# Performance work log

Measured on AMD Instinct MI355X. Metric: run time of the kernel, lower is better.

Reference implementation:

```python
import jax, jax.numpy as jnp
import numpy as np

B, S = 16, 512
IN_DIM, ATTN_DIM, DEPTH, HEADS, DH = 512, 512, 4, 8, 64
CB_DIM, CB_SIZE, MAX_SEQ = 64, 8192, 544


def _ln(x, g, b):
    mu = x.mean(-1, keepdims=True)
    v = ((x - mu) ** 2).mean(-1, keepdims=True)
    return (x - mu) / jnp.sqrt(v + 1e-5) * g + b


def setup_inputs() -> dict:
    key = jax.random.key(0)
    ks = jax.random.split(key, 16)
    sc = 0.02
    d = {
        "x": jax.random.normal(ks[0], (B, S, IN_DIM), jnp.float32),
        "w_in": jax.random.normal(ks[1], (IN_DIM, ATTN_DIM), jnp.float32) * sc,
        "b_in": jnp.zeros((ATTN_DIM,), jnp.float32),
        "pos_emb": jax.random.normal(ks[2], (MAX_SEQ, ATTN_DIM), jnp.float32) * sc,
        "ln1_g": jnp.ones((DEPTH, ATTN_DIM), jnp.float32),
        "ln1_b": jnp.zeros((DEPTH, ATTN_DIM), jnp.float32),
        "wq": jax.random.normal(ks[3], (DEPTH, ATTN_DIM, ATTN_DIM), jnp.float32) * sc,
        "wk": jax.random.normal(ks[4], (DEPTH, ATTN_DIM, ATTN_DIM), jnp.float32) * sc,
        "wv": jax.random.normal(ks[5], (DEPTH, ATTN_DIM, ATTN_DIM), jnp.float32) * sc,
        "wo": jax.random.normal(ks[6], (DEPTH, ATTN_DIM, ATTN_DIM), jnp.float32) * sc,
        "ln2_g": jnp.ones((DEPTH, ATTN_DIM), jnp.float32),
        "ln2_b": jnp.zeros((DEPTH, ATTN_DIM), jnp.float32),
        "ff_w1": jax.random.normal(ks[7], (DEPTH, ATTN_DIM, 4 * ATTN_DIM), jnp.float32) * sc,
        "ff_b1": jnp.zeros((DEPTH, 4 * ATTN_DIM), jnp.float32),
        "ff_w2": jax.random.normal(ks[8], (DEPTH, 4 * ATTN_DIM, ATTN_DIM), jnp.float32) * sc,
        "ff_b2": jnp.zeros((DEPTH, ATTN_DIM), jnp.float32),
        "lnf_g": jnp.ones((ATTN_DIM,), jnp.float32),
        "lnf_b": jnp.zeros((ATTN_DIM,), jnp.float32),
        "w_out": jax.random.normal(ks[9], (ATTN_DIM, CB_DIM), jnp.float32) * sc,
        "b_out": jnp.zeros((CB_DIM,), jnp.float32),
        "codebook": jax.random.normal(ks[10], (CB_SIZE, CB_DIM), jnp.float32),
    }
    return d


def _attn(h, wq, wk, wv, wo):
    b, s, _ = h.shape
    q = jnp.einsum('bsd,de->bse', h, wq).reshape(b, s, HEADS, DH)
    k = jnp.einsum('bsd,de->bse', h, wk).reshape(b, s, HEADS, DH)
    v = jnp.einsum('bsd,de->bse', h, wv).reshape(b, s, HEADS, DH)
    scores = jnp.einsum('bqhd,bkhd->bhqk', q, k) * (DH ** -0.5)
    a = jax.nn.softmax(scores, axis=-1)
    o = jnp.einsum('bhqk,bkhd->bqhd', a, v).reshape(b, s, ATTN_DIM)
    return jnp.einsum('bse,ed->bsd', o, wo)


def reference(x, w_in, b_in, pos_emb, ln1_g, ln1_b, wq, wk, wv, wo,
              ln2_g, ln2_b, ff_w1, ff_b1, ff_w2, ff_b2, lnf_g, lnf_b,
              w_out, b_out, codebook):
    s = x.shape[1]
    # ContinuousTransformerWrapper: project in + absolute pos emb
    h = jnp.einsum('bsd,de->bse', x, w_in) + b_in + pos_emb[:s]
    # pre-norm encoder layers: attn + ff, each residual
    for i in range(DEPTH):
        h = h + _attn(_ln(h, ln1_g[i], ln1_b[i]), wq[i], wk[i], wv[i], wo[i])
        g = _ln(h, ln2_g[i], ln2_b[i])
        g = jax.nn.gelu(jnp.einsum('bsd,df->bsf', g, ff_w1[i]) + ff_b1[i])
        h = h + jnp.einsum('bsf,fd->bsd', g, ff_w2[i]) + ff_b2[i]
    h = _ln(h, lnf_g, lnf_b)
    z = jnp.einsum('bsd,dc->bsc', h, w_out) + b_out  # [B,S,CB_DIM]
    # VectorQuantize: euclidean nearest codebook entry
    d2 = (z ** 2).sum(-1, keepdims=True) - 2.0 * jnp.einsum('bsc,kc->bsk', z, codebook) \
         + (codebook ** 2).sum(-1)  # [B,S,CB_SIZE]
    idx = jnp.argmin(d2, axis=-1)
    q = codebook[idx]  # [B,S,CB_DIM]
    commit_loss = jnp.mean((jax.lax.stop_gradient(q) - z) ** 2)  # commitment_weight=1.0
    q_st = z + jax.lax.stop_gradient(q - z)  # straight-through
    return q_st.sum(axis=1), commit_loss
```

## Files before the change

kernel.cpp:

```cpp
#include <hip/hip_runtime.h>
#include <cmath>

#define BATCH 16
#define SEQ 512
#define DMODEL 512
#define NDEPTH 4
#define NHEADS 8
#define DHEAD 64
#define DFF 2048
#define CBD 64
#define CBS 8192
#define MROWS (BATCH * SEQ)

typedef unsigned short u16;
typedef __attribute__((ext_vector_type(8))) short short8;
typedef __attribute__((ext_vector_type(4))) float f32x4;
typedef __attribute__((ext_vector_type(4))) unsigned short u16x4;

__device__ __forceinline__ u16 f2bf(float f) {
    unsigned u = __float_as_uint(f);
    u += 0x7fff + ((u >> 16) & 1);
    return (u16)(u >> 16);
}
__device__ __forceinline__ float bf2f(u16 h) {
    return __uint_as_float(((unsigned)h) << 16);
}

__device__ __forceinline__ void async16(u16* lds, const u16* g) {
    __builtin_amdgcn_global_load_lds(
        (const __attribute__((address_space(1))) unsigned int*)g,
        (__attribute__((address_space(3))) unsigned int*)lds, 16, 0, 0);
}

__device__ __forceinline__ float gelu_tanh(float u) {
    float t = fmaf(0.07135481627f * u, u * u, 1.5957691216f * u);
    return u / (1.0f + __expf(-t));
}

__global__ void zero_kernel(float* __restrict__ p, int n) {
    int i = blockIdx.x * 256 + threadIdx.x;
    if (i < n) p[i] = 0.0f;
}

__global__ void cbn_kernel(const float* __restrict__ cb, float* __restrict__ cbn) {
    int c = blockIdx.x * 256 + threadIdx.x;
    if (c >= CBS) return;
    const float* row = cb + (size_t)c * CBD;
    float s = 0.0f;
#pragma unroll
    for (int d = 0; d < CBD; ++d) s += row[d] * row[d];
    cbn[c] = s;
}

__global__ __launch_bounds__(256) void wtrans_kernel(
    const float* __restrict__ W, u16* __restrict__ Th, u16* __restrict__ Tl,
    int K, int N, long inLS, long outLS) {
    __shared__ float t[32][33];
    const float* Ws = W + (size_t)blockIdx.z * inLS;
    u16* Tho = Th + (size_t)blockIdx.z * outLS;
    u16* Tlo = Tl + (size_t)blockIdx.z * outLS;
    int n0 = blockIdx.x * 32, k0 = blockIdx.y * 32;
    int tx = threadIdx.x & 31, ty = threadIdx.x >> 5;
#pragma unroll
    for (int r = ty; r < 32; r += 8) t[r][tx] = Ws[(size_t)(k0 + r) * N + n0 + tx];
    __syncthreads();
#pragma unroll
    for (int r = ty; r < 32; r += 8) {
        float v = t[tx][r];
        size_t o = (size_t)(n0 + r) * K + k0 + tx;
        u16 hh = f2bf(v);
        Tho[o] = hh;
        Tlo[o] = f2bf(v - bf2f(hh));
    }
}

__global__ __launch_bounds__(256) void vtrans_kernel(
    const u16* __restrict__ Qh, const u16* __restrict__ Ql,
    u16* __restrict__ VTh, u16* __restrict__ VTl) {
    __shared__ u16 t[64][68];
    int s0 = blockIdx.x * 64;
    int hh = blockIdx.y;
    int b = blockIdx.z & 15, plane = blockIdx.z >> 4;
    const u16* src = (plane ? Ql : Qh) + ((size_t)(16 + hh) * MROWS) * 64;
    u16* dst = (plane ? VTl : VTh);
    int tid = threadIdx.x;
    int rr = tid >> 4, c4 = (tid & 15) * 4;
#pragma unroll
    for (int i = 0; i < 4; ++i) {
        int r = rr + i * 16;
        const u16* p = src + (size_t)(b * SEQ + s0 + r) * 64 + c4;
        *(u16x4*)(&t[r][c4]) = *(const u16x4*)p;
    }
    __syncthreads();
#pragma unroll
    for (int i = 0; i < 4; ++i) {
        int r = rr + i * 16;
        u16x4 v;
        v.x = t[c4 + 0][r]; v.y = t[c4 + 1][r]; v.z = t[c4 + 2][r]; v.w = t[c4 + 3][r];
        *(u16x4*)(dst + (size_t)b * SEQ * DMODEL + (size_t)(hh * 64 + r) * SEQ + s0 + c4) = v;
    }
}

__global__ void split_kernel(const float* __restrict__ X, u16* __restrict__ H,
                             u16* __restrict__ L, int n) {
    int i = blockIdx.x * 256 + threadIdx.x;
    if (i < n) {
        float v = X[i];
        u16 hh = f2bf(v);
        H[i] = hh;
        L[i] = f2bf(v - bf2f(hh));
    }
}

__global__ __launch_bounds__(256) void ln_kernel(
    const float* __restrict__ X,
    const float* __restrict__ C0, const float* __restrict__ C1,
    const float* __restrict__ bias2, const float* __restrict__ pos2,
    float* __restrict__ Xout,
    float* __restrict__ Y, u16* __restrict__ Yh, u16* __restrict__ Yl,
    const float* __restrict__ g, const float* __restrict__ b) {
    int row  = blockIdx.x * 4 + (threadIdx.x >> 6);
    int lane = threadIdx.x & 63;
    float v[8];
    float s = 0.0f;
#pragma unroll
    for (int j = 0; j < 8; ++j) {
        int d = lane + j * 64;
        size_t o = (size_t)row * DMODEL + d;
        float t = X ? X[o] : 0.0f;
        if (C0)    t += C0[o] + C1[o];
        if (bias2) t += bias2[d];
        if (pos2)  t += pos2[(size_t)(row & (SEQ - 1)) * DMODEL + d];
        v[j] = t;
        if (Xout) Xout[o] = t;
        s += t;
    }
#pragma unroll
    for (int off = 32; off; off >>= 1) s += __shfl_xor(s, off);
    float mu  = s * (1.0f / DMODEL);
    float var = 0.0f;
#pragma unroll
    for (int j = 0; j < 8; ++j) { float d = v[j] - mu; var += d * d; }
#pragma unroll
    for (int off = 32; off; off >>= 1) var += __shfl_xor(var, off);
    float r = rsqrtf(var * (1.0f / DMODEL) + 1e-5f);
#pragma unroll
    for (int j = 0; j < 8; ++j) {
        int d = lane + j * 64;
        float y = (v[j] - mu) * r * g[d] + b[d];
        size_t o = (size_t)row * DMODEL + d;
        if (Y) Y[o] = y;
        if (Yh) {
            u16 hh = f2bf(y);
            Yh[o] = hh;
            Yl[o] = f2bf(y - bf2f(hh));
        }
    }
}

__global__ __launch_bounds__(256) void gemm3_kernel(
    const u16* __restrict__ Ah, const u16* __restrict__ Al,
    const u16* __restrict__ Bh, const u16* __restrict__ Bl,
    float* __restrict__ Cf, u16* __restrict__ Ch, u16* __restrict__ Cl,
    const float* __restrict__ bias, const float* __restrict__ res,
    const float* __restrict__ pos, int M, int N, int K, int gelu,
    float* __restrict__ Cs0, float* __restrict__ Cs1, int kslice, int qkvscatter) {
    __shared__ __align__(16) u16 AsH[128 * 64];
    __shared__ __align__(16) u16 AsL[128 * 64];
    __shared__ __align__(16) u16 BsH[128 * 64];
    __shared__ __align__(16) u16 BsL[128 * 64];

    int tid  = threadIdx.x;
    int w    = tid >> 6, lane = tid & 63;
    int wr   = w >> 1, wc = w & 1;
    int quad = lane >> 4, l16 = lane & 15;
    int m0   = blockIdx.x * 128;
    int n0   = blockIdx.y * 128;
    int ksA  = (kslice > 0) ? blockIdx.z * kslice : 0;
    int ksB  = (kslice > 0) ? ksA + kslice : K;

    f32x4 acc[4][4];
#pragma unroll
    for (int i = 0; i < 4; ++i)
#pragma unroll
        for (int j = 0; j < 4; ++j) acc[i][j] = (f32x4){0.f, 0.f, 0.f, 0.f};

    int ldsoff[4];
    size_t goff[4];
#pragma unroll
    for (int r = 0; r < 4; ++r) {
        int cidx = tid + 256 * r;
        int row = cidx >> 3;
        int cg = (cidx & 7) ^ (row & 7);
        ldsoff[r] = cidx * 8;
        goff[r] = (size_t)row * K + cg * 8;
    }

    const u16* AbaseH = Ah + (size_t)m0 * K;
    const u16* AbaseL = Al + (size_t)m0 * K;
    const u16* BbaseH = Bh + (size_t)n0 * K;
    const u16* BbaseL = Bl + (size_t)n0 * K;

    for (int ks = ksA; ks < ksB; ks += 64) {
        __syncthreads();
#pragma unroll
        for (int r = 0; r < 4; ++r) {
            size_t g = goff[r] + ks;
            async16(&AsH[ldsoff[r]], AbaseH + g);
            async16(&AsL[ldsoff[r]], AbaseL + g);
            async16(&BsH[ldsoff[r]], BbaseH + g);
            async16(&BsL[ldsoff[r]], BbaseL + g);
        }
        __syncthreads();
#pragma unroll
        for (int s = 0; s < 2; ++s) {
            short8 afh[4], afl[4];
#pragma unroll
            for (int i = 0; i < 4; ++i) {
                int row = wr * 64 + i * 16 + l16;
                int off = row * 64 + (((s << 2) | quad) ^ (row & 7)) * 8;
                afh[i] = *(const short8*)&AsH[off];
                afl[i] = *(const short8*)&AsL[off];
            }
#pragma unroll
            for (int j = 0; j < 4; ++j) {
                int rowb = wc * 64 + j * 16 + l16;
                int offb = rowb * 64 + (((s << 2) | quad) ^ (rowb & 7)) * 8;
                short8 bh = *(const short8*)&BsH[offb];
                short8 bl = *(const short8*)&BsL[offb];
#pragma unroll
                for (int i = 0; i < 4; ++i) {
                    acc[i][j] = __builtin_amdgcn_mfma_f32_16x16x32_bf16(afh[i], bh, acc[i][j], 0, 0, 0);
                    acc[i][j] = __builtin_amdgcn_mfma_f32_16x16x32_bf16(afl[i], bh, acc[i][j], 0, 0, 0);
                    acc[i][j] = __builtin_amdgcn_mfma_f32_16x16x32_bf16(afh[i], bl, acc[i][j], 0, 0, 0);
                }
            }
        }
    }

    float* Cspl = (kslice > 0) ? (blockIdx.z ? Cs1 : Cs0) : nullptr;
    int mbase = m0 + wr * 64;
    int nbase = n0 + wc * 64;
#pragma unroll
    for (int mi = 0; mi < 4; ++mi)
#pragma unroll
        for (int ni = 0; ni < 4; ++ni) {
            f32x4 a = acc[mi][ni];
#pragma unroll
            for (int r = 0; r < 4; ++r) {
                int m = mbase + mi * 16 + quad * 4 + r;
                int n = nbase + ni * 16 + l16;
                float v = a[r];
                size_t o = qkvscatter
                    ? ((size_t)(n >> 6) * M + m) * 64 + (n & 63)
                    : (size_t)m * N + n;
                if (Cspl) { Cspl[o] = v; continue; }
                if (bias) v += bias[n];
                if (pos)  v += pos[(size_t)(m & (SEQ - 1)) * N + n];
                if (res)  v += res[(size_t)m * N + n];
                if (gelu) v = gelu_tanh(v);
                if (Cf) Cf[o] = v;
                if (Ch) {
                    u16 hh = f2bf(v);
                    Ch[o] = hh;
                    Cl[o] = f2bf(v - bf2f(hh));
                }
            }
        }
}

__global__ __launch_bounds__(256) void gemm_kernel(
    const float* __restrict__ A, const float* __restrict__ Bm,
    float* __restrict__ C, const float* __restrict__ bias,
    int M, int N, int K) {
    __shared__ float As[16][68];
    __shared__ float Bs[16][64];
    int tid = threadIdx.x;
    int tx = tid & 15, ty = tid >> 4;
    int a_m = tid >> 2, a_k = (tid & 3) * 4;
    int b_k = tid >> 4, b_n = (tid & 15) * 4;
    const float* Arow = A + (size_t)(blockIdx.x * 64 + a_m) * K;
    const float* Bcol = Bm + (size_t)blockIdx.y * 64 + b_n;
    float acc[4][4] = {};
    for (int k0 = 0; k0 < K; k0 += 16) {
        float4 av = *(const float4*)(Arow + k0 + a_k);
        float4 bv = *(const float4*)(Bcol + (size_t)(k0 + b_k) * N);
        __syncthreads();
        As[a_k + 0][a_m] = av.x; As[a_k + 1][a_m] = av.y;
        As[a_k + 2][a_m] = av.z; As[a_k + 3][a_m] = av.w;
        *(float4*)(&Bs[b_k][b_n]) = bv;
        __syncthreads();
#pragma unroll
        for (int kk = 0; kk < 16; ++kk) {
            float4 a4 = *(const float4*)(&As[kk][ty * 4]);
            float4 b4 = *(const float4*)(&Bs[kk][tx * 4]);
            float ar[4] = {a4.x, a4.y, a4.z, a4.w};
            float br[4] = {b4.x, b4.y, b4.z, b4.w};
#pragma unroll
            for (int i = 0; i < 4; ++i)
#pragma unroll
                for (int j = 0; j < 4; ++j) acc[i][j] = fmaf(ar[i], br[j], acc[i][j]);
        }
    }
    int m0 = blockIdx.x * 64 + ty * 4;
    int n0 = blockIdx.y * 64 + tx * 4;
#pragma unroll
    for (int i = 0; i < 4; ++i) {
        float vv[4];
#pragma unroll
        for (int j = 0; j < 4; ++j) {
            float t = acc[i][j];
            if (bias) t += bias[n0 + j];
            vv[j] = t;
        }
        *(float4*)(C + (size_t)(m0 + i) * N + n0) = make_float4(vv[0], vv[1], vv[2], vv[3]);
    }
}

__global__ __launch_bounds__(256) void attn_flash_kernel(
    const u16* __restrict__ QKh, const u16* __restrict__ QKl,
    const u16* __restrict__ VTh, const u16* __restrict__ VTl,
    u16* __restrict__ Oh, u16* __restrict__ Ol) {
    int bh = blockIdx.x & 127;
    int qt = blockIdx.x >> 7;
    int bb = bh >> 3, hh = bh & 7;

    __shared__ __align__(16) float Pw[4][16 * 68];
    __shared__ __align__(16) u16 KsH[64 * 64];
    __shared__ __align__(16) u16 KsL[64 * 64];
    __shared__ __align__(16) u16 VsH[64 * 64];
    __shared__ __align__(16) u16 VsL[64 * 64];

    int tid = threadIdx.x;
    int w = tid >> 6, lane = tid & 63;
    int quad = lane >> 4, l16 = lane & 15;
    int qtile = qt * 4 + w;
    float* P = Pw[w];

    const u16* qrh = QKh + ((size_t)hh * MROWS + bb * SEQ + qtile * 16 + l16) * 64 + quad * 8;
    const u16* qrl = QKl + ((size_t)hh * MROWS + bb * SEQ + qtile * 16 + l16) * 64 + quad * 8;
    short8 Qh0 = *(const short8*)qrh;
    short8 Qh1 = *(const short8*)(qrh + 32);
    short8 Ql0 = *(const short8*)qrl;
    short8 Ql1 = *(const short8*)(qrl + 32);

    float lsum[4] = {0.f, 0.f, 0.f, 0.f};
    f32x4 acc[4];
#pragma unroll
    for (int dt = 0; dt < 4; ++dt) acc[dt] = (f32x4){0.f, 0.f, 0.f, 0.f};

    const u16* KbH = QKh + ((size_t)(8 + hh) * MROWS + bb * SEQ) * 64;
    const u16* KbL = QKl + ((size_t)(8 + hh) * MROWS + bb * SEQ) * 64;
    const u16* VbH = VTh + (size_t)bb * SEQ * DMODEL + (size_t)(hh * 64) * SEQ;
    const u16* VbL = VTl + (size_t)bb * SEQ * DMODEL + (size_t)(hh * 64) * SEQ;

    int ldsoff[2];
    int goffK[2];
    size_t goffV[2];
#pragma unroll
    for (int r = 0; r < 2; ++r) {
        int cidx = tid + 256 * r;
        int row = cidx >> 3;
        int cg = (cidx & 7) ^ (row & 7);
        ldsoff[r] = cidx * 8;
        goffK[r] = row * 64 + cg * 8;
        goffV[r] = (size_t)row * SEQ + cg * 8;
    }

    for (int kt = 0; kt < 8; ++kt) {
        int kb = kt * 64;
        __syncthreads();
#pragma unroll
        for (int r = 0; r < 2; ++r) {
            async16(&KsH[ldsoff[r]], KbH + (size_t)kb * 64 + goffK[r]);
            async16(&KsL[ldsoff[r]], KbL + (size_t)kb * 64 + goffK[r]);
            async16(&VsH[ldsoff[r]], VbH + kb + goffV[r]);
            async16(&VsL[ldsoff[r]], VbL + kb + goffV[r]);
        }
        __syncthreads();

#pragma unroll
        for (int s = 0; s < 4; ++s) {
            int row = s * 16 + l16;
            int c0 = (quad ^ (row & 7)) * 8;
            int c1 = ((quad | 4) ^ (row & 7)) * 8;
            f32x4 a = (f32x4){0.f, 0.f, 0.f, 0.f};
            {
                short8 Kh0 = *(const short8*)&KsH[row * 64 + c0];
                short8 Kh1 = *(const short8*)&KsH[row * 64 + c1];
                a = __builtin_amdgcn_mfma_f32_16x16x32_bf16(Qh0, Kh0, a, 0, 0, 0);
                a = __builtin_amdgcn_mfma_f32_16x16x32_bf16(Qh1, Kh1, a, 0, 0, 0);
                a = __builtin_amdgcn_mfma_f32_16x16x32_bf16(Ql0, Kh0, a, 0, 0, 0);
                a = __builtin_amdgcn_mfma_f32_16x16x32_bf16(Ql1, Kh1, a, 0, 0, 0);
            }
            {
                short8 Kl0 = *(const short8*)&KsL[row * 64 + c0];
                short8 Kl1 = *(const short8*)&KsL[row * 64 + c1];
                a = __builtin_amdgcn_mfma_f32_16x16x32_bf16(Qh0, Kl0, a, 0, 0, 0);
                a = __builtin_amdgcn_mfma_f32_16x16x32_bf16(Qh1, Kl1, a, 0, 0, 0);
            }
#pragma unroll
            for (int r = 0; r < 4; ++r) {
                float p = __expf(a[r] * 0.125f);
                lsum[r] += p;
                P[(quad * 4 + r) * 68 + s * 16 + l16] = p;
            }
        }
#pragma unroll
        for (int ks = 0; ks < 2; ++ks) {
            short8 ph, pl;
            {
                const float* src = &P[l16 * 68 + ks * 32 + quad * 8];
                f32x4 a0 = *(const f32x4*)src;
                f32x4 a1 = *(const f32x4*)(src + 4);
                float v[8] = {a0[0], a0[1], a0[2], a0[3], a1[0], a1[1], a1[2], a1[3]};
#pragma unroll
                for (int j = 0; j < 8; ++j) {
                    u16 hv = f2bf(v[j]);
                    ph[j] = (short)hv;
                    pl[j] = (short)f2bf(v[j] - bf2f(hv));
                }
            }
#pragma unroll
            for (int dt = 0; dt < 4; ++dt) {
                int rowv = dt * 16 + l16;
                int cv = (((ks << 2) | quad) ^ (rowv & 7)) * 8;
                short8 Vh = *(const short8*)&VsH[rowv * 64 + cv];
                short8 Vl = *(const short8*)&VsL[rowv * 64 + cv];
                acc[dt] = __builtin_amdgcn_mfma_f32_16x16x32_bf16(ph, Vh, acc[dt], 0, 0, 0);
                acc[dt] = __builtin_amdgcn_mfma_f32_16x16x32_bf16(pl, Vh, acc[dt], 0, 0, 0);
                acc[dt] = __builtin_amdgcn_mfma_f32_16x16x32_bf16(ph, Vl, acc[dt], 0, 0, 0);
            }
        }
    }

#pragma unroll
    for (int r = 0; r < 4; ++r) {
#pragma unroll
        for (int off = 8; off; off >>= 1) lsum[r] += __shfl_xor(lsum[r], off);
    }
#pragma unroll
    for (int r = 0; r < 4; ++r) {
        float inv = 1.0f / lsum[r];
        size_t rowoff = (size_t)(bb * SEQ + qtile * 16 + quad * 4 + r) * DMODEL + hh * 64;
#pragma unroll
        for (int dt = 0; dt < 4; ++dt) {
            float v = acc[dt][r] * inv;
            u16 hv = f2bf(v);
            Oh[rowoff + dt * 16 + l16] = hv;
            Ol[rowoff + dt * 16 + l16] = f2bf(v - bf2f(hv));
        }
    }
}

__global__ __launch_bounds__(256) void vq3_kernel(
    const float* __restrict__ Z, const u16* __restrict__ Zh, const u16* __restrict__ Zl,
    const u16* __restrict__ CBh, const u16* __restrict__ CBl,
    const float* __restrict__ CB, const float* __restrict__ CBN,
    float* __restrict__ out) {
    __shared__ float sbest[4][16];
    __shared__ int sidx[4][16];
    __shared__ int ibest[16];
    __shared__ float psum[4][64];
    __shared__ float cl4[4];
    __shared__ __align__(16) u16 CsH[2][64 * 64];
    __shared__ __align__(16) u16 CsL[2][64 * 64];

    int tid = threadIdx.x;
    int w = tid >> 6, lane = tid & 63;
    int quad = lane >> 4, l16 = lane & 15;
    int row0 = blockIdx.x * 16;

    const u16* zph = Zh + (size_t)(row0 + l16) * CBD + quad * 8;
    const u16* zpl = Zl + (size_t)(row0 + l16) * CBD + quad * 8;
    short8 Z0h = *(const short8*)zph;
    short8 Z1h = *(const short8*)(zph + 32);
    short8 Z0l = *(const short8*)zpl;
    short8 Z1l = *(const short8*)(zpl + 32);

    float best[4] = {3.4e38f, 3.4e38f, 3.4e38f, 3.4e38f};
    int bidx[4] = {0, 0, 0, 0};

    int ldsoff[2], goffC[2];
#pragma unroll
    for (int r = 0; r < 2; ++r) {
        int cidx = tid + 256 * r;
        int row = cidx >> 3;
        int cg = (cidx & 7) ^ (row & 7);
        ldsoff[r] = cidx * 8;
        goffC[r] = row * 64 + cg * 8;
    }

    int rowc = w * 16 + l16;
    int c0 = (quad ^ (rowc & 7)) * 8;
    int c1 = ((quad | 4) ^ (rowc & 7)) * 8;

#pragma unroll
    for (int r = 0; r < 2; ++r) {
        async16(&CsH[0][ldsoff[r]], CBh + goffC[r]);
        async16(&CsL[0][ldsoff[r]], CBl + goffC[r]);
    }
    __syncthreads();

    int cur = 0;
    for (int t = 0; t < CBS; t += 64) {
        if (t + 64 < CBS) {
#pragma unroll
            for (int r = 0; r < 2; ++r) {
                async16(&CsH[cur ^ 1][ldsoff[r]], CBh + (size_t)(t + 64) * 64 + goffC[r]);
                async16(&CsL[cur ^ 1][ldsoff[r]], CBl + (size_t)(t + 64) * 64 + goffC[r]);
            }
        }

        int code = t + rowc;
        short8 C0h = *(const short8*)&CsH[cur][rowc * 64 + c0];
        short8 C1h = *(const short8*)&CsH[cur][rowc * 64 + c1];
        short8 C0l = *(const short8*)&CsL[cur][rowc * 64 + c0];
        short8 C1l = *(const short8*)&CsL[cur][rowc * 64 + c1];
        float cn = CBN[code];
        f32x4 a = (f32x4){0.f, 0.f, 0.f, 0.f};
        a = __builtin_amdgcn_mfma_f32_16x16x32_bf16(Z0h, C0h, a, 0, 0, 0);
        a = __builtin_amdgcn_mfma_f32_16x16x32_bf16(Z1h, C1h, a, 0, 0, 0);
        a = __builtin_amdgcn_mfma_f32_16x16x32_bf16(Z0l, C0h, a, 0, 0, 0);
        a = __builtin_amdgcn_mfma_f32_16x16x32_bf16(Z1l, C1h, a, 0, 0, 0);
        a = __builtin_amdgcn_mfma_f32_16x16x32_bf16(Z0h, C0l, a, 0, 0, 0);
        a = __builtin_amdgcn_mfma_f32_16x16x32_bf16(Z1h, C1l, a, 0, 0, 0);
#pragma unroll
        for (int r = 0; r < 4; ++r) {
            float s = cn - 2.0f * a[r];
            if (s < best[r]) { best[r] = s; bidx[r] = code; }
        }

        __syncthreads();
        cur ^= 1;
    }

#pragma unroll
    for (int off = 8; off; off >>= 1) {
#pragma unroll
        for (int r = 0; r < 4; ++r) {
            float ov = __shfl_xor(best[r], off);
            int oi = __shfl_xor(bidx[r], off);
            if (ov < best[r] || (ov == best[r] && oi < bidx[r])) { best[r] = ov; bidx[r] = oi; }
        }
    }
    if (l16 == 0) {
#pragma unroll
        for (int r = 0; r < 4; ++r) {
            sbest[w][quad * 4 + r] = best[r];
            sidx[w][quad * 4 + r] = bidx[r];
        }
    }
    __syncthreads();
    if (tid < 16) {
        float bv = sbest[0][tid];
        int bi = sidx[0][tid];
#pragma unroll
        for (int ww = 1; ww < 4; ++ww) {
            float ov = sbest[ww][tid];
            int oi = sidx[ww][tid];
            if (ov < bv || (ov == bv && oi < bi)) { bv = ov; bi = oi; }
        }
        ibest[tid] = bi;
    }
    __syncthreads();

    int d2 = lane;
    float qacc = 0.0f, closs = 0.0f;
#pragma unroll
    for (int j = 0; j < 4; ++j) {
        int r2 = w * 4 + j;
        int bi = ibest[r2];
        float q = CB[(size_t)bi * CBD + d2];
        float z = Z[(size_t)(row0 + r2) * CBD + d2];
        qacc += q;
        float df = q - z;
        closs += df * df;
    }
    psum[w][d2] = qacc;
#pragma unroll
    for (int off = 32; off; off >>= 1) closs += __shfl_xor(closs, off);
    if (d2 == 0) cl4[w] = closs;
    __syncthreads();
    if (tid < 64) {
        float t = psum[0][tid] + psum[1][tid] + psum[2][tid] + psum[3][tid];
        int b = row0 >> 9;
        atomicAdd(out + b * 64 + tid, t);
    }
    if (tid == 0)
        atomicAdd(out + 1024, (cl4[0] + cl4[1] + cl4[2] + cl4[3]) * (1.0f / (float)(MROWS * CBD)));
}

extern "C" void kernel_launch(void* const* d_in, const int* in_sizes, int n_in,
                              void* d_out, int out_size, void* d_ws, size_t ws_size,
                              hipStream_t stream) {
    const float* x    = (const float*)d_in[0];
    const float* w_in = (const float*)d_in[1];
    const float* b_in = (const float*)d_in[2];
    const float* pos  = (const float*)d_in[3];
    const float* ln1g = (const float*)d_in[4];
    const float* ln1b = (const float*)d_in[5];
    const float* wq   = (const float*)d_in[6];
    const float* wk   = (const float*)d_in[7];
    const float* wv   = (const float*)d_in[8];
    const float* wo   = (const float*)d_in[9];
    const float* ln2g = (const float*)d_in[10];
    const float* ln2b = (const float*)d_in[11];
    const float* ffw1 = (const float*)d_in[12];
    const float* ffb1 = (const float*)d_in[13];
    const float* ffw2 = (const float*)d_in[14];
    const float* ffb2 = (const float*)d_in[15];
    const float* lnfg = (const float*)d_in[16];
    const float* lnfb = (const float*)d_in[17];
    const float* wout = (const float*)d_in[18];
    const float* bout = (const float*)d_in[19];
    const float* cb   = (const float*)d_in[20];
    float* out = (float*)d_out;

    const size_t MD  = (size_t)MROWS * DMODEL;
    const size_t MQ  = (size_t)MROWS * 1536;
    const size_t MF  = (size_t)MROWS * DFF;

    float* ws   = (float*)d_ws;
    float* h    = ws;
    float* t0   = h + MD;
    float* big  = t0 + MD;
    float* zb   = big + MF;
    float* cbn  = zb + (size_t)MROWS * CBD;
    u16* cbh    = (u16*)(cbn + CBS);
    u16* cbl    = cbh + (size_t)CBS * CBD;
    u16* t0h    = (u16*)(cbh + 2 * (size_t)CBS * CBD);
    u16* t0l    = t0h + MD;
    u16* wb     = t0l + MD;

    u16* qkvh = (u16*)big;
    u16* qkvl = qkvh + MQ;
    u16* obh  = qkvl + MQ;
    u16* obl  = obh + MD;
    u16* xh   = obh;
    u16* xl   = obl;
    u16* fmh  = (u16*)big;
    u16* fml  = fmh + MF;
    u16* zbh  = (u16*)big;
    u16* zbl  = zbh + (size_t)MROWS * CBD;

    const size_t S_WIN  = (size_t)DMODEL * DMODEL;
    const size_t S_QKV  = (size_t)1536 * DMODEL * NDEPTH;
    const size_t S_WO   = S_WIN * NDEPTH;
    const size_t S_FF1  = (size_t)DFF * DMODEL * NDEPTH;
    const size_t S_FF2  = S_FF1;
    u16* winT_h = wb;
    u16* winT_l = winT_h + S_WIN;
    u16* qkvT_h = winT_l + S_WIN;
    u16* qkvT_l = qkvT_h + S_QKV;
    u16* woT_h  = qkvT_l + S_QKV;
    u16* woT_l  = woT_h + S_WO;
    u16* ff1T_h = woT_l + S_WO;
    u16* ff1T_l = ff1T_h + S_FF1;
    u16* ff2T_h = ff1T_l + S_FF1;
    u16* ff2T_l = ff2T_h + S_FF2;
    u16* VTh = ff2T_l + S_FF2;
    u16* VTl = VTh + (size_t)BATCH * SEQ * DMODEL;
    float* spK0 = (float*)(VTl + (size_t)BATCH * SEQ * DMODEL);
    float* spK1 = spK0 + MD;

    dim3 blk(256);

    zero_kernel<<<dim3((out_size + 255) / 256), blk, 0, stream>>>(out, out_size);
    cbn_kernel<<<dim3(CBS / 256), blk, 0, stream>>>(cb, cbn);
    split_kernel<<<dim3((int)(CBS * CBD / 256)), blk, 0, stream>>>(cb, cbh, cbl, CBS * CBD);

    wtrans_kernel<<<dim3(16, 16, 1), blk, 0, stream>>>(w_in, winT_h, winT_l, DMODEL, DMODEL, 0, 0);
    wtrans_kernel<<<dim3(16, 16, NDEPTH), blk, 0, stream>>>(
        wq, qkvT_h, qkvT_l, DMODEL, DMODEL, (long)DMODEL * DMODEL, (long)1536 * DMODEL);
    wtrans_kernel<<<dim3(16, 16, NDEPTH), blk, 0, stream>>>(
        wk, qkvT_h + (size_t)512 * DMODEL, qkvT_l + (size_t)512 * DMODEL,
        DMODEL, DMODEL, (long)DMODEL * DMODEL, (long)1536 * DMODEL);
    wtrans_kernel<<<dim3(16, 16, NDEPTH), blk, 0, stream>>>(
        wv, qkvT_h + (size_t)1024 * DMODEL, qkvT_l + (size_t)1024 * DMODEL,
        DMODEL, DMODEL, (long)DMODEL * DMODEL, (long)1536 * DMODEL);
    wtrans_kernel<<<dim3(16, 16, NDEPTH), blk, 0, stream>>>(
        wo, woT_h, woT_l, DMODEL, DMODEL, (long)DMODEL * DMODEL, (long)DMODEL * DMODEL);
    wtrans_kernel<<<dim3(DFF / 32, 16, NDEPTH), blk, 0, stream>>>(
        ffw1, ff1T_h, ff1T_l, DMODEL, DFF, (long)DMODEL * DFF, (long)DFF * DMODEL);
    wtrans_kernel<<<dim3(16, DFF / 32, NDEPTH), blk, 0, stream>>>(
        ffw2, ff2T_h, ff2T_l, DFF, DMODEL, (long)DFF * DMODEL, (long)DMODEL * DFF);

    split_kernel<<<dim3((int)(MD / 256)), blk, 0, stream>>>(x, xh, xl, (int)MD);

    gemm3_kernel<<<dim3(MROWS / 128, DMODEL / 128, 2), blk, 0, stream>>>(
        xh, xl, winT_h, winT_l, nullptr, nullptr, nullptr, nullptr, nullptr, nullptr,
        MROWS, DMODEL, DMODEL, 0, spK0, spK1, 256, 0);

    for (int l = 0; l < NDEPTH; ++l) {
        ln_kernel<<<dim3(MROWS / 4), blk, 0, stream>>>(
            (l == 0) ? nullptr : h, spK0, spK1,
            (l == 0) ? b_in : (ffb2 + (size_t)(l - 1) * DMODEL),
            (l == 0) ? pos : nullptr, h,
            nullptr, t0h, t0l, ln1g + l * DMODEL, ln1b + l * DMODEL);
        gemm3_kernel<<<dim3(MROWS / 128, 1536 / 128, 1), blk, 0, stream>>>(
            t0h, t0l, qkvT_h + (size_t)l * 1536 * DMODEL, qkvT_l + (size_t)l * 1536 * DMODEL,
            nullptr, qkvh, qkvl, nullptr, nullptr, nullptr, MROWS, 1536, DMODEL, 0,
            nullptr, nullptr, 0, 1);
        vtrans_kernel<<<dim3(8, 8, 32), blk, 0, stream>>>(qkvh, qkvl, VTh, VTl);
        attn_flash_kernel<<<dim3(1024), blk, 0, stream>>>(
            qkvh, qkvl, VTh, VTl, obh, obl);
        gemm3_kernel<<<dim3(MROWS / 128, DMODEL / 128, 2), blk, 0, stream>>>(
            obh, obl, woT_h + (size_t)l * S_WIN, woT_l + (size_t)l * S_WIN,
            nullptr, nullptr, nullptr, nullptr, nullptr, nullptr,
            MROWS, DMODEL, DMODEL, 0, spK0, spK1, 256, 0);
        ln_kernel<<<dim3(MROWS / 4), blk, 0, stream>>>(
            h, spK0, spK1, nullptr, nullptr, h,
            nullptr, t0h, t0l, ln2g + l * DMODEL, ln2b + l * DMODEL);
        gemm3_kernel<<<dim3(MROWS / 128, DFF / 128, 1), blk, 0, stream>>>(
            t0h, t0l, ff1T_h + (size_t)l * DFF * DMODEL, ff1T_l + (size_t)l * DFF * DMODEL,
            nullptr, fmh, fml, ffb1 + l * DFF, nullptr, nullptr, MROWS, DFF, DMODEL, 1,
            nullptr, nullptr, 0, 0);
        gemm3_kernel<<<dim3(MROWS / 128, DMODEL / 128, 2), blk, 0, stream>>>(
            fmh, fml, ff2T_h + (size_t)l * DFF * DMODEL, ff2T_l + (size_t)l * DFF * DMODEL,
            nullptr, nullptr, nullptr, nullptr, nullptr, nullptr,
            MROWS, DMODEL, DFF, 0, spK0, spK1, 1024, 0);
    }

    ln_kernel<<<dim3(MROWS / 4), blk, 0, stream>>>(
        h, spK0, spK1, ffb2 + (size_t)3 * DMODEL, nullptr, nullptr,
        t0, nullptr, nullptr, lnfg, lnfb);
    gemm_kernel<<<dim3(MROWS / 64, 1), blk, 0, stream>>>(t0, wout, zb, bout, MROWS, CBD, DMODEL);
    split_kernel<<<dim3((int)((size_t)MROWS * CBD / 256)), blk, 0, stream>>>(
        zb, zbh, zbl, MROWS * CBD);
    vq3_kernel<<<dim3(MROWS / 16), blk, 0, stream>>>(zb, zbh, zbl, cbh, cbl, cb, cbn, out);
}
```

Baseline: 1.472 ms.

## Double-buffer GEMM K-tiles and widen VQ codebook tile to 128 codes

The split-bf16 GEMM now uses two 32-wide K buffers in shared memory. The next tile is prefetched asynchronously while MFMAs run on the current one, replacing the old load-then-compute pattern that had two barriers per 64-wide step. The VQ kernel processes 128 codebook entries per iteration with two interleaved accumulator chains, which halves the barrier count and gives the MFMA pipeline independent work. The costs are more LDS use in VQ, which may lower occupancy, and more iterations with smaller tiles in the GEMM. Both changes keep the same total shared memory for the GEMM.

```diff
diff --git a/kernel.cpp b/kernel.cpp
--- a/kernel.cpp
+++ b/kernel.cpp
@@ -165,10 +165,10 @@
     const float* __restrict__ bias, const float* __restrict__ res,
     const float* __restrict__ pos, int M, int N, int K, int gelu,
     float* __restrict__ Cs0, float* __restrict__ Cs1, int kslice, int qkvscatter) {
-    __shared__ __align__(16) u16 AsH[128 * 64];
-    __shared__ __align__(16) u16 AsL[128 * 64];
-    __shared__ __align__(16) u16 BsH[128 * 64];
-    __shared__ __align__(16) u16 BsL[128 * 64];
+    __shared__ __align__(16) u16 AsH[2][128 * 32];
+    __shared__ __align__(16) u16 AsL[2][128 * 32];
+    __shared__ __align__(16) u16 BsH[2][128 * 32];
+    __shared__ __align__(16) u16 BsL[2][128 * 32];
 
     int tid  = threadIdx.x;
     int w    = tid >> 6, lane = tid & 63;
@@ -185,13 +185,13 @@
 #pragma unroll
         for (int j = 0; j < 4; ++j) acc[i][j] = (f32x4){0.f, 0.f, 0.f, 0.f};
 
-    int ldsoff[4];
-    size_t goff[4];
-#pragma unroll
-    for (int r = 0; r < 4; ++r) {
+    int ldsoff[2];
+    size_t goff[2];
+#pragma unroll
+    for (int r = 0; r < 2; ++r) {
         int cidx = tid + 256 * r;
-        int row = cidx >> 3;
-        int cg = (cidx & 7) ^ (row & 7);
+        int row = cidx >> 2;
+        int cg = (cidx & 3) ^ (row & 3);
         ldsoff[r] = cidx * 8;
         goff[r] = (size_t)row * K + cg * 8;
     }
@@ -201,41 +201,60 @@
     const u16* BbaseH = Bh + (size_t)n0 * K;
     const u16* BbaseL = Bl + (size_t)n0 * K;
 
-    for (int ks = ksA; ks < ksB; ks += 64) {
+    int nks = (ksB - ksA) >> 5;
+
+#pragma unroll
+    for (int r = 0; r < 2; ++r) {
+        size_t g = goff[r] + ksA;
+        async16(&AsH[0][ldsoff[r]], AbaseH + g);
+        async16(&AsL[0][ldsoff[r]], AbaseL + g);
+        async16(&BsH[0][ldsoff[r]], BbaseH + g);
+        async16(&BsL[0][ldsoff[r]], BbaseL + g);
+    }
+    __syncthreads();
+
+    int cur = 0;
+    for (int s2 = 0; s2 < nks; ++s2) {
+        if (s2 + 1 < nks) {
+            int kn = ksA + (s2 + 1) * 32;
+#pragma unroll
+            for (int r = 0; r < 2; ++r) {
+                size_t g = goff[r] + kn;
+                async16(&AsH[cur ^ 1][ldsoff[r]], AbaseH + g);
+                async16(&AsL[cur ^ 1][ldsoff[r]], AbaseL + g);
+                async16(&BsH[cur ^ 1][ldsoff[r]], BbaseH + g);
+                async16(&BsL[cur ^ 1][ldsoff[r]], BbaseL + g);
+            }
+        }
+
+        const u16* asH = AsH[cur];
+        const u16* asL = AsL[cur];
+        const u16* bsH = BsH[cur];
+        const u16* bsL = BsL[cur];
+        short8 afh[4], afl[4];
+#pragma unroll
+        for (int i = 0; i < 4; ++i) {
+            int row = wr * 64 + i * 16 + l16;
+            int off = row * 32 + ((quad ^ (row & 3)) * 8);
+            afh[i] = *(const short8*)&asH[off];
+            afl[i] = *(const short8*)&asL[off];
+        }
+#pragma unroll
+        for (int j = 0; j < 4; ++j) {
+            int rowb = wc * 64 + j * 16 + l16;
+            int offb = rowb * 32 + ((quad ^ (rowb & 3)) * 8);
+            short8 bh = *(const short8*)&bsH[offb];
+            short8 bl = *(const short8*)&bsL[offb];
+#pragma unroll
+            for (int i = 0; i < 4; ++i) {
+                acc[i][j] = __builtin_amdgcn_mfma_f32_16x16x32_bf16(afh[i], bh, acc[i][j], 0, 0, 0);
+                acc[i][j] = __builtin_amdgcn_mfma_f32_16x16x32_bf16(afl[i], bh, acc[i][j], 0, 0, 0);
+                acc[i][j] = __builtin_amdgcn_mfma_f32_16x16x32_bf16(afh[i], bl, acc[i][j], 0, 0, 0);
+            }
+        }
+
         __syncthreads();
-#pragma unroll
-        for (int r = 0; r < 4; ++r) {
-            size_t g = goff[r] + ks;
-            async16(&AsH[ldsoff[r]], AbaseH + g);
-            async16(&AsL[ldsoff[r]], AbaseL + g);
-            async16(&BsH[ldsoff[r]], BbaseH + g);
-            async16(&BsL[ldsoff[r]], BbaseL + g);
-        }
-        __syncthreads();
-#pragma unroll
-        for (int s = 0; s < 2; ++s) {
-            short8 afh[4], afl[4];
-#pragma unroll
-            for (int i = 0; i < 4; ++i) {
-                int row = wr * 64 + i * 16 + l16;
-                int off = row * 64 + (((s << 2) | quad) ^ (row & 7)) * 8;
-                afh[i] = *(const short8*)&AsH[off];
-                afl[i] = *(const short8*)&AsL[off];
-            }
-#pragma unroll
-            for (int j = 0; j < 4; ++j) {
-                int rowb = wc * 64 + j * 16 + l16;
-                int offb = rowb * 64 + (((s << 2) | quad) ^ (rowb & 7)) * 8;
-                short8 bh = *(const short8*)&BsH[offb];
-                short8 bl = *(const short8*)&BsL[offb];
-#pragma unroll
-                for (int i = 0; i < 4; ++i) {
-                    acc[i][j] = __builtin_amdgcn_mfma_f32_16x16x32_bf16(afh[i], bh, acc[i][j], 0, 0, 0);
-                    acc[i][j] = __builtin_amdgcn_mfma_f32_16x16x32_bf16(afl[i], bh, acc[i][j], 0, 0, 0);
-                    acc[i][j] = __builtin_amdgcn_mfma_f32_16x16x32_bf16(afh[i], bl, acc[i][j], 0, 0, 0);
-                }
-            }
-        }
+        cur ^= 1;
     }
 
     float* Cspl = (kslice > 0) ? (blockIdx.z ? Cs1 : Cs0) : nullptr;
@@ -463,8 +482,8 @@
     __shared__ int ibest[16];
     __shared__ float psum[4][64];
     __shared__ float cl4[4];
-    __shared__ __align__(16) u16 CsH[2][64 * 64];
-    __shared__ __align__(16) u16 CsL[2][64 * 64];
+    __shared__ __align__(16) u16 CsH[2][128 * 64];
+    __shared__ __align__(16) u16 CsL[2][128 * 64];
 
     int tid = threadIdx.x;
     int w = tid >> 6, lane = tid & 63;
@@ -481,9 +500,9 @@
     float best[4] = {3.4e38f, 3.4e38f, 3.4e38f, 3.4e38f};
     int bidx[4] = {0, 0, 0, 0};
 
-    int ldsoff[2], goffC[2];
-#pragma unroll
-    for (int r = 0; r < 2; ++r) {
+    int ldsoff[4], goffC[4];
+#pragma unroll
+    for (int r = 0; r < 4; ++r) {
         int cidx = tid + 256 * r;
         int row = cidx >> 3;
         int cg = (cidx & 7) ^ (row & 7);
@@ -491,44 +510,64 @@
         goffC[r] = row * 64 + cg * 8;
     }
 
-    int rowc = w * 16 + l16;
-    int c0 = (quad ^ (rowc & 7)) * 8;
-    int c1 = ((quad | 4) ^ (rowc & 7)) * 8;
-
-#pragma unroll
-    for (int r = 0; r < 2; ++r) {
+    int rowc0 = w * 16 + l16;
+    int rowc1 = rowc0 + 64;
+    int a0c0 = (quad ^ (rowc0 & 7)) * 8;
+    int a0c1 = ((quad | 4) ^ (rowc0 & 7)) * 8;
+    int a1c0 = (quad ^ (rowc1 & 7)) * 8;
+    int a1c1 = ((quad | 4) ^ (rowc1 & 7)) * 8;
+
+#pragma unroll
+    for (int r = 0; r < 4; ++r) {
         async16(&CsH[0][ldsoff[r]], CBh + goffC[r]);
         async16(&CsL[0][ldsoff[r]], CBl + goffC[r]);
     }
     __syncthreads();
 
     int cur = 0;
-    for (int t = 0; t < CBS; t += 64) {
-        if (t + 64 < CBS) {
-#pragma unroll
-            for (int r = 0; r < 2; ++r) {
-                async16(&CsH[cur ^ 1][ldsoff[r]], CBh + (size_t)(t + 64) * 64 + goffC[r]);
-                async16(&CsL[cur ^ 1][ldsoff[r]], CBl + (size_t)(t + 64) * 64 + goffC[r]);
-            }
-        }
-
-        int code = t + rowc;
-        short8 C0h = *(const short8*)&CsH[cur][rowc * 64 + c0];
-        short8 C1h = *(const short8*)&CsH[cur][rowc * 64 + c1];
-        short8 C0l = *(const short8*)&CsL[cur][rowc * 64 + c0];
-        short8 C1l = *(const short8*)&CsL[cur][rowc * 64 + c1];
-        float cn = CBN[code];
-        f32x4 a = (f32x4){0.f, 0.f, 0.f, 0.f};
-        a = __builtin_amdgcn_mfma_f32_16x16x32_bf16(Z0h, C0h, a, 0, 0, 0);
-        a = __builtin_amdgcn_mfma_f32_16x16x32_bf16(Z1h, C1h, a, 0, 0, 0);
-        a = __builtin_amdgcn_mfma_f32_16x16x32_bf16(Z0l, C0h, a, 0, 0, 0);
-        a = __builtin_amdgcn_mfma_f32_16x16x32_bf16(Z1l, C1h, a, 0, 0, 0);
-        a = __builtin_amdgcn_mfma_f32_16x16x32_bf16(Z0h, C0l, a, 0, 0, 0);
-        a = __builtin_amdgcn_mfma_f32_16x16x32_bf16(Z1h, C1l, a, 0, 0, 0);
+    for (int t = 0; t < CBS; t += 128) {
+        if (t + 128 < CBS) {
+#pragma unroll
+            for (int r = 0; r < 4; ++r) {
+                async16(&CsH[cur ^ 1][ldsoff[r]], CBh + (size_t)(t + 128) * 64 + goffC[r]);
+                async16(&CsL[cur ^ 1][ldsoff[r]], CBl + (size_t)(t + 128) * 64 + goffC[r]);
+            }
+        }
+
+        int code0 = t + rowc0;
+        int code1 = t + rowc1;
+        const u16* csH = CsH[cur];
+        const u16* csL = CsL[cur];
+        short8 A0h = *(const short8*)&csH[rowc0 * 64 + a0c0];
+        short8 A1h = *(const short8*)&csH[rowc0 * 64 + a0c1];
+        short8 A0l = *(const short8*)&csL[rowc0 * 64 + a0c0];
+        short8 A1l = *(const short8*)&csL[rowc0 * 64 + a0c1];
+        short8 B0h = *(const short8*)&csH[rowc1 * 64 + a1c0];
+        short8 B1h = *(const short8*)&csH[rowc1 * 64 + a1c1];
+        short8 B0l = *(const short8*)&csL[rowc1 * 64 + a1c0];
+        short8 B1l = *(const short8*)&csL[rowc1 * 64 + a1c1];
+        float cnA = CBN[code0];
+        float cnB = CBN[code1];
+        f32x4 aA = (f32x4){0.f, 0.f, 0.f, 0.f};
+        f32x4 aB = (f32x4){0.f, 0.f, 0.f, 0.f};
+        aA = __builtin_amdgcn_mfma_f32_16x16x32_bf16(Z0h, A0h, aA, 0, 0, 0);
+        aB = __builtin_amdgcn_mfma_f32_16x16x32_bf16(Z0h, B0h, aB, 0, 0, 0);
+        aA = __builtin_amdgcn_mfma_f32_16x16x32_bf16(Z1h, A1h, aA, 0, 0, 0);
+        aB = __builtin_amdgcn_mfma_f32_16x16x32_bf16(Z1h, B1h, aB, 0, 0, 0);
+        aA = __builtin_amdgcn_mfma_f32_16x16x32_bf16(Z0l, A0h, aA, 0, 0, 0);
+        aB = __builtin_amdgcn_mfma_f32_16x16x32_bf16(Z0l, B0h, aB, 0, 0, 0);
+        aA = __builtin_amdgcn_mfma_f32_16x16x32_bf16(Z1l, A1h, aA, 0, 0, 0);
+        aB = __builtin_amdgcn_mfma_f32_16x16x32_bf16(Z1l, B1h, aB, 0, 0, 0);
+        aA = __builtin_amdgcn_mfma_f32_16x16x32_bf16(Z0h, A0l, aA, 0, 0, 0);
+        aB = __builtin_amdgcn_mfma_f32_16x16x32_bf16(Z0h, B0l, aB, 0, 0, 0);
+        aA = __builtin_amdgcn_mfma_f32_16x16x32_bf16(Z1h, A1l, aA, 0, 0, 0);
+        aB = __builtin_amdgcn_mfma_f32_16x16x32_bf16(Z1h, B1l, aB, 0, 0, 0);
 #pragma unroll
         for (int r = 0; r < 4; ++r) {
-            float s = cn - 2.0f * a[r];
-            if (s < best[r]) { best[r] = s; bidx[r] = code; }
+            float sA = cnA - 2.0f * aA[r];
+            if (sA < best[r]) { best[r] = sA; bidx[r] = code0; }
+            float sB = cnB - 2.0f * aB[r];
+            if (sB < best[r]) { best[r] = sB; bidx[r] = code1; }
         }
 
         __syncthreads();
```

After: 1.584 ms. 1.08x slower.
